# Performance work log

Measured on AMD Instinct MI355X. Metric: run time of the kernel, lower is better.

The kernel has to match this reference:

```python
import jax, jax.numpy as jnp
import numpy as np

N = 50000      # nodes
E = 800000     # edges (avg degree 16)
F_IN = 64      # node_features (== GENConv out, so no input projection)
H = 64         # hidden
EXP = 2 * H    # GENConv MLP expansion dim = 128
D2 = F_IN + H  # dense-block concat dim = SAGEConv in = 128
EPS_MSG = 1e-7 # GENConv message eps
BN_EPS = 1e-5


def setup_inputs() -> dict:
    key = jax.random.key(0)
    ks = jax.random.split(key, 16)
    g = lambda k, shape, fan: jax.random.normal(k, shape, jnp.float32) / np.sqrt(fan)
    return {
        "x": jax.random.normal(ks[0], (N, F_IN), jnp.float32),
        "edge_index": jax.random.randint(ks[1], (2, E), 0, N, jnp.int32),
        # GENConv MLP: Linear(64,128) -> BatchNorm(128) -> ReLU -> Linear(128,64)
        "W1": g(ks[2], (H, EXP), H), "b1": jnp.zeros((EXP,), jnp.float32),
        "gamma": jnp.ones((EXP,), jnp.float32), "beta": jnp.zeros((EXP,), jnp.float32),
        "W2": g(ks[3], (EXP, H), EXP), "b2": jnp.zeros((H,), jnp.float32),
        # SAGEConv project Linear(128,128), lin_l Linear(128,64), lin_r Linear(128,64,bias=False)
        "Wp": g(ks[4], (D2, D2), D2), "bp": jnp.zeros((D2,), jnp.float32),
        "Wl": g(ks[5], (D2, H), D2), "bl": jnp.zeros((H,), jnp.float32),
        "Wr": g(ks[6], (D2, H), D2),
        # fc Linear(64,1)
        "Wf": g(ks[7], (H, 1), H), "bf": jnp.zeros((1,), jnp.float32),
    }


def _forward(x, W1, b1, gamma, beta, W2, b2, Wp, bp, Wl, bl, Wr, Wf, bf, src, dst):
    n = x.shape[0]
    # ---- GENConv(aggr='softmax', t=1.0): msg = relu(x_j) + eps -------------
    msg = jax.nn.relu(x[src]) + EPS_MSG                       # [E, H]
    mmax = jax.ops.segment_max(msg, dst, num_segments=n)      # per-dst, per-feature max
    mmax = jax.lax.stop_gradient(jnp.where(jnp.isfinite(mmax), mmax, 0.0))
    e = jnp.exp(msg - mmax[dst])                              # t = 1.0
    denom = jax.ops.segment_sum(e, dst, num_segments=n)
    numer = jax.ops.segment_sum(e * msg, dst, num_segments=n)
    agg = numer / jnp.where(denom > 0, denom, 1.0)            # softmax aggregation
    out = agg + x                                             # residual with x_dst
    # GENConv MLP (BatchNorm in training mode: batch stats, biased var)
    h = out @ W1 + b1
    mu = h.mean(axis=0)
    var = h.var(axis=0)
    h = (h - mu) * jax.lax.rsqrt(var + BN_EPS) * gamma + beta
    h = jax.nn.relu(h) @ W2 + b2                              # [N, H]
    # ---- DeepGCNLayer block='dense': concat input ---------------------------
    x2 = jnp.concatenate([x, h], axis=-1)                     # [N, F_IN+H]
    x2 = jax.nn.sigmoid(x2)                                   # self.relu = Sigmoid()
    # ---- SAGEConv(project=True, aggr=DeepSetsAggregation()==sum) -----------
    xp = jax.nn.relu(x2 @ Wp + bp)                            # projected source feats
    aggr = jax.ops.segment_sum(xp[src], dst, num_segments=n)  # DeepSets w/o nns = sum
    out2 = aggr @ Wl + bl + x2 @ Wr                           # root uses UNprojected x2
    out2 = jax.nn.sigmoid(out2)
    logits = out2 @ Wf + bf                                   # [N, 1]
    probs = jax.nn.sigmoid(logits)                            # training branch
    return probs, logits


def reference(x, edge_index, W1, b1, gamma, beta, W2, b2, Wp, bp, Wl, bl, Wr, Wf, bf):
    src, dst = edge_index[0], edge_index[1]
    return _forward(x, W1, b1, gamma, beta, W2, b2, Wp, bp, Wl, bl, Wr, Wf, bf, src, dst)
```

## Files before the change

### kernel.cpp

```cpp
#include <hip/hip_runtime.h>

#define F_IN 64
#define HID 64
#define EXPD 128
#define D2 128
#define MAXDEG 64
#define NBW 128
#define NB 391
#define NBINB 98
#define SUBCAP 64
#define EPT 32

typedef __attribute__((ext_vector_type(8))) short bf16x8;
typedef __attribute__((ext_vector_type(4))) float f32x4;

__device__ __forceinline__ float sigmoidf_(float x) {
    return 1.0f / (1.0f + __expf(-x));
}
__device__ __forceinline__ unsigned bf16rne_(float f) {
    unsigned u = __float_as_uint(f);
    return (u + 0x7FFFu + ((u >> 16) & 1u)) >> 16;
}
__device__ __forceinline__ float bf16tof_(unsigned u16) {
    return __uint_as_float(u16 << 16);
}

__global__ __launch_bounds__(256) void k_bin(const int* __restrict__ ei,
                                             int* __restrict__ cnt2,
                                             unsigned* __restrict__ binned2,
                                             const float* __restrict__ x,
                                             unsigned short* __restrict__ x16,
                                             const float* __restrict__ W1,
                                             const float* __restrict__ W2,
                                             const float* __restrict__ Wp,
                                             const float* __restrict__ Wl,
                                             const float* __restrict__ Wr,
                                             short* __restrict__ dst,
                                             float* __restrict__ bnsums,
                                             int nE, int n, int nbinb) {
    int b = blockIdx.x;
    int tid = threadIdx.x;
    if (b < nbinb) {
        __shared__ int hist[NB];
        if (b == 0) bnsums[tid] = 0.f;
        for (int i = tid; i < NB; i += 256) hist[i] = 0;
        __syncthreads();
        unsigned ed[EPT];
        unsigned short rk[EPT];
        int e0 = b * (256 * EPT);
#pragma unroll
        for (int j = 0; j < EPT; ++j) {
            int e = e0 + j * 256 + tid;
            if (e < nE) {
                unsigned s = (unsigned)ei[e];
                unsigned d = (unsigned)ei[nE + e];
                ed[j] = s | (d << 16);
                rk[j] = (unsigned short)atomicAdd(&hist[d >> 7], 1);
            }
        }
        __syncthreads();
        for (int i = tid; i < NB; i += 256) cnt2[b * NB + i] = hist[i];
#pragma unroll
        for (int j = 0; j < EPT; ++j) {
            int e = e0 + j * 256 + tid;
            if (e < nE) {
                int bin = (ed[j] >> 16) >> 7;
                int r = (int)rk[j];
                if (r < SUBCAP)
                    binned2[((size_t)bin * nbinb + b) * SUBCAP + r] = ed[j];
            }
        }
        return;
    }
    b -= nbinb;
    if (b < 192) {
        int e = b * 256 + tid;
        const float* src;
        int K, N, base2;
        if (e < 8192)       { src = W1; K = 64;  N = 128; base2 = 0; }
        else if (e < 16384) { src = W2; K = 128; N = 64;  base2 = 8192; }
        else if (e < 32768) { src = Wp; K = 128; N = 128; base2 = 16384; }
        else if (e < 40960) { src = Wl; K = 128; N = 64;  base2 = 32768; }
        else                { src = Wr; K = 128; N = 64;  base2 = 40960; }
        int le = e - base2;
        int j = le & 7;
        int lane = (le >> 3) & 63;
        int n16 = lane & 15, q = lane >> 4;
        int rest = le >> 9;
        int KC = K / 32;
        int kc = rest % KC, nt = rest / KC;
        int k = kc * 32 + q * 8 + j;
        int col = nt * 16 + n16;
        dst[e] = (short)bf16rne_(src[(size_t)k * N + col]);
        return;
    }
    int i0 = (b - 192) * 1024 + tid * 4;
    if (i0 < n * F_IN) {
        float4 v = *(const float4*)(x + i0);
        uint2 pk;
        pk.x = bf16rne_(v.x) | (bf16rne_(v.y) << 16);
        pk.y = bf16rne_(v.z) | (bf16rne_(v.w) << 16);
        *(uint2*)(x16 + i0) = pk;
    }
}

__global__ __launch_bounds__(256) void k_csr(const int* __restrict__ cnt2,
                                             const unsigned* __restrict__ binned2,
                                             int* __restrict__ counts,
                                             unsigned short* __restrict__ csr,
                                             int n, int nbinb) {
    __shared__ unsigned short lcsr[NBW * MAXDEG];
    __shared__ int lcnt[NBW];
    __shared__ int scnt[NBINB];
    int b = blockIdx.x;
    int tid = threadIdx.x;
    if (tid < NBW) lcnt[tid] = 0;
    for (int i = tid; i < nbinb; i += 256) {
        int c = cnt2[i * NB + b];
        scnt[i] = c < SUBCAP ? c : SUBCAP;
    }
    __syncthreads();
    const unsigned* src = binned2 + (size_t)b * nbinb * SUBCAP;
    int tot = nbinb * SUBCAP;
    for (int i = tid; i < tot; i += 256) {
        int blk = i >> 6;
        int r = i & (SUBCAP - 1);
        if (r < scnt[blk]) {
            unsigned u = src[i];
            int dl = (int)(u >> 16) - b * NBW;
            int slot = atomicAdd(&lcnt[dl], 1);
            if (slot < MAXDEG) lcsr[dl * MAXDEG + slot] = (unsigned short)(u & 0xFFFF);
        }
    }
    __syncthreads();
    int nodebase = b * NBW;
    if (tid < NBW && nodebase + tid < n) counts[nodebase + tid] = lcnt[tid];
    int nrows = n - nodebase;
    nrows = nrows < NBW ? nrows : NBW;
    int nu4 = nrows * 8;
    uint4* dstrow = (uint4*)(csr + (size_t)nodebase * MAXDEG);
    for (int idx = tid; idx < nu4; idx += 256) dstrow[idx] = ((const uint4*)lcsr)[idx];
}

__global__ __launch_bounds__(1024) void k_geng(const unsigned short* __restrict__ x16,
                                               const int* __restrict__ counts,
                                               const unsigned short* __restrict__ csr,
                                               const short* __restrict__ Wf,
                                               const float* __restrict__ b1,
                                               unsigned short* __restrict__ h16,
                                               float* __restrict__ bnsums, int n) {
    __shared__ short As[64 * 64];
    __shared__ float bnred[256];
    const unsigned* x32 = (const unsigned*)x16;
    int tid = threadIdx.x;
    int w = tid >> 6;
    int lane = tid & 63;
    int H = lane >> 5, f2 = lane & 31;
    int rblk = blockIdx.x * 64;
    if (tid < 256) bnred[tid] = 0.f;
    for (int t = 0; t < 4; ++t) {
        int rr = w * 4 + t;
        int v = rblk + rr;
        int q8 = f2 >> 2;
        int slot = ((rr >> 4) * 2 + (q8 >> 2)) * 64 + (q8 & 3) * 16 + (rr & 15);
        if (v < n) {
            int deg = counts[v];
            deg = deg > MAXDEG ? MAXDEG : deg;
            int idx = 0;
            if (lane < deg) idx = (int)csr[(size_t)v * MAXDEG + lane];
            float d0 = 0.f, d1 = 0.f, n0 = 0.f, n1 = 0.f;
            int i = 0;
            for (; i + 16 <= deg; i += 16) {
                unsigned us[8];
#pragma unroll
                for (int tt = 0; tt < 8; ++tt) {
                    int s = __shfl(idx, i + tt * 2 + H, 64);
                    us[tt] = x32[(size_t)s * 32 + f2];
                }
#pragma unroll
                for (int tt = 0; tt < 8; ++tt) {
                    unsigned u = us[tt];
                    float m0 = fmaxf(bf16tof_(u & 0xFFFF), 0.f) + 1e-7f;
                    float m1 = fmaxf(bf16tof_(u >> 16), 0.f) + 1e-7f;
                    float e0 = __expf(m0), e1 = __expf(m1);
                    d0 += e0; d1 += e1;
                    n0 = fmaf(e0, m0, n0);
                    n1 = fmaf(e1, m1, n1);
                }
            }
            for (; i + 8 <= deg; i += 8) {
                int sA = __shfl(idx, i + 0 + H, 64);
                int sB = __shfl(idx, i + 2 + H, 64);
                int sC = __shfl(idx, i + 4 + H, 64);
                int sD = __shfl(idx, i + 6 + H, 64);
                unsigned uA = x32[(size_t)sA * 32 + f2];
                unsigned uB = x32[(size_t)sB * 32 + f2];
                unsigned uC = x32[(size_t)sC * 32 + f2];
                unsigned uD = x32[(size_t)sD * 32 + f2];
#pragma unroll
                for (int tt = 0; tt < 4; ++tt) {
                    unsigned u = tt == 0 ? uA : tt == 1 ? uB : tt == 2 ? uC : uD;
                    float m0 = fmaxf(bf16tof_(u & 0xFFFF), 0.f) + 1e-7f;
                    float m1 = fmaxf(bf16tof_(u >> 16), 0.f) + 1e-7f;
                    float e0 = __expf(m0), e1 = __expf(m1);
                    d0 += e0; d1 += e1;
                    n0 = fmaf(e0, m0, n0);
                    n1 = fmaf(e1, m1, n1);
                }
            }
            for (; i + 2 <= deg; i += 2) {
                int s = __shfl(idx, i + H, 64);
                unsigned u = x32[(size_t)s * 32 + f2];
                float m0 = fmaxf(bf16tof_(u & 0xFFFF), 0.f) + 1e-7f;
                float m1 = fmaxf(bf16tof_(u >> 16), 0.f) + 1e-7f;
                float e0 = __expf(m0), e1 = __expf(m1);
                d0 += e0; d1 += e1;
                n0 = fmaf(e0, m0, n0);
                n1 = fmaf(e1, m1, n1);
            }
            if (i < deg) {
                int s = __shfl(idx, i, 64);
                if (H == 0) {
                    unsigned u = x32[(size_t)s * 32 + f2];
                    float m0 = fmaxf(bf16tof_(u & 0xFFFF), 0.f) + 1e-7f;
                    float m1 = fmaxf(bf16tof_(u >> 16), 0.f) + 1e-7f;
                    float e0 = __expf(m0), e1 = __expf(m1);
                    d0 += e0; d1 += e1;
                    n0 = fmaf(e0, m0, n0);
                    n1 = fmaf(e1, m1, n1);
                }
            }
            d0 += __shfl_xor(d0, 32, 64);
            d1 += __shfl_xor(d1, 32, 64);
            n0 += __shfl_xor(n0, 32, 64);
            n1 += __shfl_xor(n1, 32, 64);
            if (H == 0) {
                float a0 = (deg > 0) ? (n0 / d0) : 0.f;
                float a1 = (deg > 0) ? (n1 / d1) : 0.f;
                unsigned xv = x32[(size_t)v * 32 + f2];
                float r0 = a0 + bf16tof_(xv & 0xFFFF);
                float r1 = a1 + bf16tof_(xv >> 16);
                *(unsigned*)(As + slot * 8 + (f2 & 3) * 2) =
                    bf16rne_(r0) | (bf16rne_(r1) << 16);
            }
        } else {
            if (H == 0) *(unsigned*)(As + slot * 8 + (f2 & 3) * 2) = 0u;
        }
    }
    __syncthreads();
    int L = lane;
    int q = L >> 4, n16 = L & 15;
    int mt = w & 3;
    int nt_base = (w >> 2) * 2;
    f32x4 acc[2];
#pragma unroll
    for (int nt = 0; nt < 2; ++nt) acc[nt] = (f32x4){0.f, 0.f, 0.f, 0.f};
#pragma unroll
    for (int kc = 0; kc < 2; ++kc) {
        bf16x8 a = *(const bf16x8*)(As + ((mt * 2 + kc) * 64 + L) * 8);
#pragma unroll
        for (int nt = 0; nt < 2; ++nt) {
            bf16x8 b = *(const bf16x8*)(Wf + (size_t)(((nt_base + nt) * 2 + kc) * 64 + L) * 8);
            acc[nt] = __builtin_amdgcn_mfma_f32_16x16x32_bf16(a, b, acc[nt], 0, 0, 0);
        }
    }
#pragma unroll
    for (int nt = 0; nt < 2; ++nt) {
        int col = (nt_base + nt) * 16 + n16;
        float bv = b1[col];
        float s = 0.f, s2 = 0.f;
#pragma unroll
        for (int r = 0; r < 4; ++r) {
            int row = rblk + mt * 16 + q * 4 + r;
            float hv = acc[nt][r] + bv;
            if (row < n) {
                h16[(size_t)row * EXPD + col] = (unsigned short)bf16rne_(hv);
                s += hv;
                s2 = fmaf(hv, hv, s2);
            }
        }
        s += __shfl_xor(s, 16, 64);
        s += __shfl_xor(s, 32, 64);
        s2 += __shfl_xor(s2, 16, 64);
        s2 += __shfl_xor(s2, 32, 64);
        if (q == 0) {
            atomicAdd(&bnred[col], s);
            atomicAdd(&bnred[128 + col], s2);
        }
    }
    __syncthreads();
    if (tid < 256) atomicAdd(&bnsums[tid], bnred[tid]);
}

__global__ __launch_bounds__(256) void k_mlp2ab(const unsigned short* __restrict__ h16,
                                                const float* __restrict__ bnsums,
                                                const float* __restrict__ gamma,
                                                const float* __restrict__ beta,
                                                const short* __restrict__ Wf2,
                                                const float* __restrict__ b2,
                                                const unsigned short* __restrict__ x16,
                                                const short* __restrict__ Wfp,
                                                const short* __restrict__ Wfl,
                                                const short* __restrict__ Wfr,
                                                const float* __restrict__ bp,
                                                unsigned short* __restrict__ yp16,
                                                unsigned short* __restrict__ yr16,
                                                float inv_n, int n) {
    __shared__ short Bs[64 * 128];
    __shared__ short As[64 * 128];
    __shared__ float ssl[256];
    int tid = threadIdx.x;
    int rblk = blockIdx.x * 64;
    if (tid < 128) {
        float mu = bnsums[tid] * inv_n;
        float var = fmaf(-mu, mu, bnsums[128 + tid] * inv_n);
        float rs = rsqrtf(fmaxf(var, 0.f) + 1e-5f);
        float scale = gamma[tid] * rs;
        ssl[tid] = scale;
        ssl[128 + tid] = fmaf(-mu, scale, beta[tid]);
    }
    __syncthreads();
#pragma unroll
    for (int it = 0; it < 4; ++it) {
        int c = it * 256 + tid;
        int rr = c & 63, q8 = c >> 6;
        int gr = rblk + rr;
        gr = gr < n ? gr : n - 1;
        uint4 v = *(const uint4*)(h16 + (size_t)gr * EXPD + q8 * 8);
        float4 sc1 = *(const float4*)(ssl + q8 * 8);
        float4 sc2 = *(const float4*)(ssl + q8 * 8 + 4);
        float4 sh1 = *(const float4*)(ssl + 128 + q8 * 8);
        float4 sh2 = *(const float4*)(ssl + 128 + q8 * 8 + 4);
        float o0 = fmaxf(fmaf(bf16tof_(v.x & 0xFFFF), sc1.x, sh1.x), 0.f);
        float o1 = fmaxf(fmaf(bf16tof_(v.x >> 16),    sc1.y, sh1.y), 0.f);
        float o2 = fmaxf(fmaf(bf16tof_(v.y & 0xFFFF), sc1.z, sh1.z), 0.f);
        float o3 = fmaxf(fmaf(bf16tof_(v.y >> 16),    sc1.w, sh1.w), 0.f);
        float o4 = fmaxf(fmaf(bf16tof_(v.z & 0xFFFF), sc2.x, sh2.x), 0.f);
        float o5 = fmaxf(fmaf(bf16tof_(v.z >> 16),    sc2.y, sh2.y), 0.f);
        float o6 = fmaxf(fmaf(bf16tof_(v.w & 0xFFFF), sc2.z, sh2.z), 0.f);
        float o7 = fmaxf(fmaf(bf16tof_(v.w >> 16),    sc2.w, sh2.w), 0.f);
        uint4 pk;
        pk.x = bf16rne_(o0) | (bf16rne_(o1) << 16);
        pk.y = bf16rne_(o2) | (bf16rne_(o3) << 16);
        pk.z = bf16rne_(o4) | (bf16rne_(o5) << 16);
        pk.w = bf16rne_(o6) | (bf16rne_(o7) << 16);
        int slot = ((rr >> 4) * 4 + (q8 >> 2)) * 64 + (q8 & 3) * 16 + (rr & 15);
        *(uint4*)(Bs + slot * 8) = pk;
    }
#pragma unroll
    for (int it = 0; it < 2; ++it) {
        int c = it * 256 + tid;
        int rr = c & 63, q8 = c >> 6;
        int gr = rblk + rr;
        gr = gr < n ? gr : n - 1;
        uint4 v = *(const uint4*)(x16 + (size_t)gr * F_IN + q8 * 8);
        float o0 = sigmoidf_(bf16tof_(v.x & 0xFFFF));
        float o1 = sigmoidf_(bf16tof_(v.x >> 16));
        float o2 = sigmoidf_(bf16tof_(v.y & 0xFFFF));
        float o3 = sigmoidf_(bf16tof_(v.y >> 16));
        float o4 = sigmoidf_(bf16tof_(v.z & 0xFFFF));
        float o5 = sigmoidf_(bf16tof_(v.z >> 16));
        float o6 = sigmoidf_(bf16tof_(v.w & 0xFFFF));
        float o7 = sigmoidf_(bf16tof_(v.w >> 16));
        uint4 pk;
        pk.x = bf16rne_(o0) | (bf16rne_(o1) << 16);
        pk.y = bf16rne_(o2) | (bf16rne_(o3) << 16);
        pk.z = bf16rne_(o4) | (bf16rne_(o5) << 16);
        pk.w = bf16rne_(o6) | (bf16rne_(o7) << 16);
        int slot = ((rr >> 4) * 4 + (q8 >> 2)) * 64 + (q8 & 3) * 16 + (rr & 15);
        *(uint4*)(As + slot * 8) = pk;
    }
    __syncthreads();
    int L = tid & 63, w = tid >> 6;
    int q = L >> 4, n16 = L & 15;
    {
        int mtb = (w & 1) * 2, ntb = (w >> 1) * 2;
        f32x4 acch[2][2];
#pragma unroll
        for (int mt = 0; mt < 2; ++mt)
#pragma unroll
            for (int nt = 0; nt < 2; ++nt) acch[mt][nt] = (f32x4){0.f, 0.f, 0.f, 0.f};
#pragma unroll
        for (int kc = 0; kc < 4; ++kc) {
            bf16x8 a0 = *(const bf16x8*)(Bs + (((mtb + 0) * 4 + kc) * 64 + L) * 8);
            bf16x8 a1 = *(const bf16x8*)(Bs + (((mtb + 1) * 4 + kc) * 64 + L) * 8);
#pragma unroll
            for (int nt = 0; nt < 2; ++nt) {
                bf16x8 b = *(const bf16x8*)(Wf2 + (size_t)(((ntb + nt) * 4 + kc) * 64 + L) * 8);
                acch[0][nt] = __builtin_amdgcn_mfma_f32_16x16x32_bf16(a0, b, acch[0][nt], 0, 0, 0);
                acch[1][nt] = __builtin_amdgcn_mfma_f32_16x16x32_bf16(a1, b, acch[1][nt], 0, 0, 0);
            }
        }
#pragma unroll
        for (int nt = 0; nt < 2; ++nt) {
            int col = (ntb + nt) * 16 + n16;
            float bv = b2[col];
            int q8b = 8 + (col >> 3), jb = col & 7;
#pragma unroll
            for (int mt = 0; mt < 2; ++mt)
#pragma unroll
                for (int r = 0; r < 4; ++r) {
                    int rr2 = (w & 1) * 32 + mt * 16 + q * 4 + r;
                    float hv = sigmoidf_(acch[mt][nt][r] + bv);
                    int slot = ((rr2 >> 4) * 4 + (q8b >> 2)) * 64 + (q8b & 3) * 16 + (rr2 & 15);
                    As[slot * 8 + jb] = (short)bf16rne_(hv);
                }
        }
    }
    __syncthreads();
    int mt_base = (w & 1) * 2;
    int nt_base = (w >> 1) * 4;
    f32x4 acc[2][4];
    f32x4 accr[2][2];
#pragma unroll
    for (int mt = 0; mt < 2; ++mt) {
#pragma unroll
        for (int nt = 0; nt < 4; ++nt) acc[mt][nt] = (f32x4){0.f, 0.f, 0.f, 0.f};
#pragma unroll
        for (int nt = 0; nt < 2; ++nt) accr[mt][nt] = (f32x4){0.f, 0.f, 0.f, 0.f};
    }
#pragma unroll
    for (int kc = 0; kc < 4; ++kc) {
        bf16x8 a0 = *(const bf16x8*)(As + (((mt_base + 0) * 4 + kc) * 64 + L) * 8);
        bf16x8 a1 = *(const bf16x8*)(As + (((mt_base + 1) * 4 + kc) * 64 + L) * 8);
#pragma unroll
        for (int nt = 0; nt < 4; ++nt) {
            bf16x8 b = *(const bf16x8*)(Wfp + (size_t)(((nt_base + nt) * 4 + kc) * 64 + L) * 8);
            acc[0][nt] = __builtin_amdgcn_mfma_f32_16x16x32_bf16(a0, b, acc[0][nt], 0, 0, 0);
            acc[1][nt] = __builtin_amdgcn_mfma_f32_16x16x32_bf16(a1, b, acc[1][nt], 0, 0, 0);
        }
#pragma unroll
        for (int nt = 0; nt < 2; ++nt) {
            bf16x8 b = *(const bf16x8*)(Wfr + (size_t)((((w >> 1) * 2 + nt) * 4 + kc) * 64 + L) * 8);
            accr[0][nt] = __builtin_amdgcn_mfma_f32_16x16x32_bf16(a0, b, accr[0][nt], 0, 0, 0);
            accr[1][nt] = __builtin_amdgcn_mfma_f32_16x16x32_bf16(a1, b, accr[1][nt], 0, 0, 0);
        }
    }
#pragma unroll
    for (int nt = 0; nt < 2; ++nt) {
        int col = ((w >> 1) * 2 + nt) * 16 + n16;
#pragma unroll
        for (int mt = 0; mt < 2; ++mt)
#pragma unroll
            for (int r = 0; r < 4; ++r) {
                int row = rblk + (w & 1) * 32 + mt * 16 + q * 4 + r;
                if (row < n)
                    yr16[(size_t)row * HID + col] = (unsigned short)bf16rne_(accr[mt][nt][r]);
            }
    }
#pragma unroll
    for (int nt = 0; nt < 4; ++nt) {
        int kk = (nt_base + nt) * 16 + n16;
        float bv = bp[kk];
        int q8b = kk >> 3, jb = kk & 7;
#pragma unroll
        for (int mt = 0; mt < 2; ++mt)
#pragma unroll
            for (int r = 0; r < 4; ++r) {
                int rr2 = (w & 1) * 32 + mt * 16 + q * 4 + r;
                float xv = fmaxf(acc[mt][nt][r] + bv, 0.f);
                int slot = ((rr2 >> 4) * 4 + (q8b >> 2)) * 64 + (q8b & 3) * 16 + (rr2 & 15);
                Bs[slot * 8 + jb] = (short)bf16rne_(xv);
            }
    }
    __syncthreads();
    f32x4 acc2[4];
#pragma unroll
    for (int nt = 0; nt < 4; ++nt) acc2[nt] = (f32x4){0.f, 0.f, 0.f, 0.f};
#pragma unroll
    for (int kc = 0; kc < 4; ++kc) {
        bf16x8 a = *(const bf16x8*)(Bs + ((w * 4 + kc) * 64 + L) * 8);
#pragma unroll
        for (int nt = 0; nt < 4; ++nt) {
            bf16x8 b = *(const bf16x8*)(Wfl + (size_t)((nt * 4 + kc) * 64 + L) * 8);
            acc2[nt] = __builtin_amdgcn_mfma_f32_16x16x32_bf16(a, b, acc2[nt], 0, 0, 0);
        }
    }
#pragma unroll
    for (int nt = 0; nt < 4; ++nt) {
        int col = nt * 16 + n16;
#pragma unroll
        for (int r = 0; r < 4; ++r) {
            int row = rblk + w * 16 + q * 4 + r;
            if (row < n)
                yp16[(size_t)row * HID + col] = (unsigned short)bf16rne_(acc2[nt][r]);
        }
    }
}

__global__ __launch_bounds__(256) void k_sagef(const unsigned short* __restrict__ yp16,
                                               const int* __restrict__ counts,
                                               const unsigned short* __restrict__ csr,
                                               const unsigned short* __restrict__ yr16,
                                               const float* __restrict__ bl,
                                               const float* __restrict__ Wfv,
                                               const float* __restrict__ bf,
                                               float* __restrict__ out, int n) {
    const unsigned* yp32 = (const unsigned*)yp16;
    int wid = threadIdx.x >> 6;
    int lane = threadIdx.x & 63;
    int H = lane >> 5, f2 = lane & 31;
    int v = blockIdx.x * 4 + wid;
    if (v >= n) return;
    int deg = counts[v];
    deg = deg > MAXDEG ? MAXDEG : deg;
    int idx = 0;
    if (lane < deg) idx = (int)csr[(size_t)v * MAXDEG + lane];
    float a0 = 0.f, a1 = 0.f;
    int i = 0;
    for (; i + 16 <= deg; i += 16) {
        unsigned us[8];
#pragma unroll
        for (int tt = 0; tt < 8; ++tt) {
            int s = __shfl(idx, i + tt * 2 + H, 64);
            us[tt] = yp32[(size_t)s * 32 + f2];
        }
#pragma unroll
        for (int tt = 0; tt < 8; ++tt) {
            a0 += bf16tof_(us[tt] & 0xFFFF);
            a1 += bf16tof_(us[tt] >> 16);
        }
    }
    for (; i + 8 <= deg; i += 8) {
        int sA = __shfl(idx, i + 0 + H, 64);
        int sB = __shfl(idx, i + 2 + H, 64);
        int sC = __shfl(idx, i + 4 + H, 64);
        int sD = __shfl(idx, i + 6 + H, 64);
        unsigned uA = yp32[(size_t)sA * 32 + f2];
        unsigned uB = yp32[(size_t)sB * 32 + f2];
        unsigned uC = yp32[(size_t)sC * 32 + f2];
        unsigned uD = yp32[(size_t)sD * 32 + f2];
        a0 += bf16tof_(uA & 0xFFFF) + bf16tof_(uB & 0xFFFF) +
              bf16tof_(uC & 0xFFFF) + bf16tof_(uD & 0xFFFF);
        a1 += bf16tof_(uA >> 16) + bf16tof_(uB >> 16) +
              bf16tof_(uC >> 16) + bf16tof_(uD >> 16);
    }
    for (; i + 2 <= deg; i += 2) {
        int s = __shfl(idx, i + H, 64);
        unsigned u = yp32[(size_t)s * 32 + f2];
        a0 += bf16tof_(u & 0xFFFF);
        a1 += bf16tof_(u >> 16);
    }
    if (i < deg) {
        int s = __shfl(idx, i, 64);
        if (H == 0) {
            unsigned u = yp32[(size_t)s * 32 + f2];
            a0 += bf16tof_(u & 0xFFFF);
            a1 += bf16tof_(u >> 16);
        }
    }
    a0 += __shfl_xor(a0, 32, 64);
    a1 += __shfl_xor(a1, 32, 64);
    if (H == 0) {
        unsigned u = ((const unsigned*)yr16)[(size_t)v * 32 + f2];
        float2 blv = ((const float2*)bl)[f2];
        float2 wv  = ((const float2*)Wfv)[f2];
        float o0 = sigmoidf_(a0 + blv.x + bf16tof_(u & 0xFFFF));
        float o1 = sigmoidf_(a1 + blv.y + bf16tof_(u >> 16));
        float t = fmaf(o0, wv.x, o1 * wv.y);
        t += __shfl_xor(t, 1, 64);
        t += __shfl_xor(t, 2, 64);
        t += __shfl_xor(t, 4, 64);
        t += __shfl_xor(t, 8, 64);
        t += __shfl_xor(t, 16, 64);
        if (f2 == 0) {
            float lg = t + bf[0];
            out[v] = sigmoidf_(lg);
            out[n + v] = lg;
        }
    }
}

extern "C" void kernel_launch(void* const* d_in, const int* in_sizes, int n_in,
                              void* d_out, int out_size, void* d_ws, size_t ws_size,
                              hipStream_t stream) {
    const float* x     = (const float*)d_in[0];
    const int*   ei    = (const int*)d_in[1];
    const float* W1    = (const float*)d_in[2];
    const float* b1    = (const float*)d_in[3];
    const float* gamma = (const float*)d_in[4];
    const float* beta  = (const float*)d_in[5];
    const float* W2    = (const float*)d_in[6];
    const float* b2    = (const float*)d_in[7];
    const float* Wp    = (const float*)d_in[8];
    const float* bp    = (const float*)d_in[9];
    const float* Wl    = (const float*)d_in[10];
    const float* bl    = (const float*)d_in[11];
    const float* Wr    = (const float*)d_in[12];
    const float* Wfv   = (const float*)d_in[13];
    const float* bf    = (const float*)d_in[14];
    const int n = in_sizes[0] / F_IN;
    const int e = in_sizes[1] / 2;

    char* ws = (char*)d_ws;
    size_t off = 0;
    auto alloc = [&](size_t bytes) -> void* {
        void* p = (void*)(ws + off);
        off += (bytes + 255) & ~(size_t)255;
        return p;
    };
    const int nbinb = (e + 256 * EPT - 1) / (256 * EPT);
    float*          bnsums   = (float*)alloc(256 * 4);
    int*            cnt2     = (int*)alloc((size_t)nbinb * NB * 4);
    int*            counts   = (int*)alloc((size_t)n * 4);
    unsigned short* csr      = (unsigned short*)alloc((size_t)n * MAXDEG * 2);
    unsigned*       binned2  = (unsigned*)alloc((size_t)NB * nbinb * SUBCAP * 4);
    unsigned short* x16      = (unsigned short*)alloc((size_t)n * F_IN * 2);
    unsigned short* h16      = (unsigned short*)alloc((size_t)n * EXPD * 2);
    unsigned short* yp16     = (unsigned short*)alloc((size_t)n * HID * 2);
    unsigned short* yr16     = (unsigned short*)alloc((size_t)n * HID * 2);
    short*          wfrag    = (short*)alloc(49152 * 2);

    float* out = (float*)d_out;
    const int nb64  = (n + 63) / 64;
    const int nb4   = (n + 3) / 4;
    const int nfp = nbinb + 192 + ((n * F_IN + 1023) / 1024);

    k_bin<<<nfp, 256, 0, stream>>>(ei, cnt2, binned2, x, x16, W1, W2, Wp, Wl,
                                   Wr, wfrag, bnsums, e, n, nbinb);
    k_csr<<<NB, 256, 0, stream>>>(cnt2, binned2, counts, csr, n, nbinb);
    k_geng<<<nb64, 1024, 0, stream>>>(x16, counts, csr, wfrag, b1, h16, bnsums, n);
    k_mlp2ab<<<nb64, 256, 0, stream>>>(h16, bnsums, gamma, beta, wfrag + 8192, b2,
                                       x16, wfrag + 16384, wfrag + 32768,
                                       wfrag + 40960, bp, yp16, yr16,
                                       1.0f / (float)n, n);
    k_sagef<<<nb4, 256, 0, stream>>>(yp16, counts, csr, yr16, bl, Wfv, bf, out, n);
}
```

Before: 209.5 us.

## Fuse CSR construction into GENConv gather kernel using 64-node bins

Removes the separate k_csr kernel. Each 64-row k_geng block now builds its own node neighbor lists in shared memory from the binned edge buckets, reads degrees and sources from LDS, and also writes counts and CSR out for the later SAGE kernel. Bin width drops from 128 to 64 nodes so the bins line up with the GEMM row blocks, and the per-sub-bucket capacity shrinks from 64 to 40. This saves one launch and the CSR global round trip before the gather. In exchange the gather kernel carries extra shared memory and work before it starts, and a sub-bucket that overflows 40 entries would silently drop edges.

```diff
diff --git a/kernel.cpp b/kernel.cpp
--- a/kernel.cpp
+++ b/kernel.cpp
@@ -5,10 +5,9 @@
 #define EXPD 128
 #define D2 128
 #define MAXDEG 64
-#define NBW 128
-#define NB 391
+#define NB 782
 #define NBINB 98
-#define SUBCAP 64
+#define SUBCAP 40
 #define EPT 32
 
 typedef __attribute__((ext_vector_type(8))) short bf16x8;
@@ -55,7 +54,7 @@
                 unsigned s = (unsigned)ei[e];
                 unsigned d = (unsigned)ei[nE + e];
                 ed[j] = s | (d << 16);
-                rk[j] = (unsigned short)atomicAdd(&hist[d >> 7], 1);
+                rk[j] = (unsigned short)atomicAdd(&hist[d >> 6], 1);
             }
         }
         __syncthreads();
@@ -64,7 +63,7 @@
         for (int j = 0; j < EPT; ++j) {
             int e = e0 + j * 256 + tid;
             if (e < nE) {
-                int bin = (ed[j] >> 16) >> 7;
+                int bin = (ed[j] >> 16) >> 6;
                 int r = (int)rk[j];
                 if (r < SUBCAP)
                     binned2[((size_t)bin * nbinb + b) * SUBCAP + r] = ed[j];
@@ -104,51 +103,19 @@
     }
 }
 
-__global__ __launch_bounds__(256) void k_csr(const int* __restrict__ cnt2,
-                                             const unsigned* __restrict__ binned2,
-                                             int* __restrict__ counts,
-                                             unsigned short* __restrict__ csr,
-                                             int n, int nbinb) {
-    __shared__ unsigned short lcsr[NBW * MAXDEG];
-    __shared__ int lcnt[NBW];
-    __shared__ int scnt[NBINB];
-    int b = blockIdx.x;
-    int tid = threadIdx.x;
-    if (tid < NBW) lcnt[tid] = 0;
-    for (int i = tid; i < nbinb; i += 256) {
-        int c = cnt2[i * NB + b];
-        scnt[i] = c < SUBCAP ? c : SUBCAP;
-    }
-    __syncthreads();
-    const unsigned* src = binned2 + (size_t)b * nbinb * SUBCAP;
-    int tot = nbinb * SUBCAP;
-    for (int i = tid; i < tot; i += 256) {
-        int blk = i >> 6;
-        int r = i & (SUBCAP - 1);
-        if (r < scnt[blk]) {
-            unsigned u = src[i];
-            int dl = (int)(u >> 16) - b * NBW;
-            int slot = atomicAdd(&lcnt[dl], 1);
-            if (slot < MAXDEG) lcsr[dl * MAXDEG + slot] = (unsigned short)(u & 0xFFFF);
-        }
-    }
-    __syncthreads();
-    int nodebase = b * NBW;
-    if (tid < NBW && nodebase + tid < n) counts[nodebase + tid] = lcnt[tid];
-    int nrows = n - nodebase;
-    nrows = nrows < NBW ? nrows : NBW;
-    int nu4 = nrows * 8;
-    uint4* dstrow = (uint4*)(csr + (size_t)nodebase * MAXDEG);
-    for (int idx = tid; idx < nu4; idx += 256) dstrow[idx] = ((const uint4*)lcsr)[idx];
-}
-
-__global__ __launch_bounds__(1024) void k_geng(const unsigned short* __restrict__ x16,
-                                               const int* __restrict__ counts,
-                                               const unsigned short* __restrict__ csr,
+__global__ __launch_bounds__(1024) void k_geng(const int* __restrict__ cnt2,
+                                               const unsigned* __restrict__ binned2,
+                                               const unsigned short* __restrict__ x16,
                                                const short* __restrict__ Wf,
                                                const float* __restrict__ b1,
                                                unsigned short* __restrict__ h16,
-                                               float* __restrict__ bnsums, int n) {
+                                               float* __restrict__ bnsums,
+                                               int* __restrict__ counts,
+                                               unsigned short* __restrict__ csr,
+                                               int n, int nbinb) {
+    __shared__ unsigned short lcsr[64 * MAXDEG];
+    __shared__ int lcnt[64];
+    __shared__ int scnt[NBINB];
     __shared__ short As[64 * 64];
     __shared__ float bnred[256];
     const unsigned* x32 = (const unsigned*)x16;
@@ -156,18 +123,46 @@
     int w = tid >> 6;
     int lane = tid & 63;
     int H = lane >> 5, f2 = lane & 31;
-    int rblk = blockIdx.x * 64;
+    int b = blockIdx.x;
+    int rblk = b * 64;
+    if (tid < 64) lcnt[tid] = 0;
     if (tid < 256) bnred[tid] = 0.f;
+    for (int i = tid; i < nbinb; i += 1024) {
+        int c = cnt2[i * NB + b];
+        scnt[i] = c < SUBCAP ? c : SUBCAP;
+    }
+    __syncthreads();
+    const unsigned* esrc = binned2 + (size_t)b * nbinb * SUBCAP;
+    int tot = nbinb * SUBCAP;
+    for (int i = tid; i < tot; i += 1024) {
+        int blk = i / SUBCAP;
+        int r = i - blk * SUBCAP;
+        if (r < scnt[blk]) {
+            unsigned u = esrc[i];
+            int dl = (int)(u >> 16) - rblk;
+            int slot = atomicAdd(&lcnt[dl], 1);
+            if (slot < MAXDEG) lcsr[dl * MAXDEG + slot] = (unsigned short)(u & 0xFFFF);
+        }
+    }
+    __syncthreads();
+    if (tid < 64 && rblk + tid < n) counts[rblk + tid] = lcnt[tid];
+    {
+        int nrows = n - rblk;
+        nrows = nrows < 64 ? nrows : 64;
+        int nu4 = nrows * 8;
+        uint4* dstrow = (uint4*)(csr + (size_t)rblk * MAXDEG);
+        for (int i = tid; i < nu4; i += 1024) dstrow[i] = ((const uint4*)lcsr)[i];
+    }
     for (int t = 0; t < 4; ++t) {
         int rr = w * 4 + t;
         int v = rblk + rr;
         int q8 = f2 >> 2;
         int slot = ((rr >> 4) * 2 + (q8 >> 2)) * 64 + (q8 & 3) * 16 + (rr & 15);
         if (v < n) {
-            int deg = counts[v];
+            int deg = lcnt[rr];
             deg = deg > MAXDEG ? MAXDEG : deg;
             int idx = 0;
-            if (lane < deg) idx = (int)csr[(size_t)v * MAXDEG + lane];
+            if (lane < deg) idx = (int)lcsr[rr * MAXDEG + lane];
             float d0 = 0.f, d1 = 0.f, n0 = 0.f, n1 = 0.f;
             int i = 0;
             for (; i + 16 <= deg; i += 16) {
@@ -260,8 +255,8 @@
         bf16x8 a = *(const bf16x8*)(As + ((mt * 2 + kc) * 64 + L) * 8);
 #pragma unroll
         for (int nt = 0; nt < 2; ++nt) {
-            bf16x8 b = *(const bf16x8*)(Wf + (size_t)(((nt_base + nt) * 2 + kc) * 64 + L) * 8);
-            acc[nt] = __builtin_amdgcn_mfma_f32_16x16x32_bf16(a, b, acc[nt], 0, 0, 0);
+            bf16x8 b2 = *(const bf16x8*)(Wf + (size_t)(((nt_base + nt) * 2 + kc) * 64 + L) * 8);
+            acc[nt] = __builtin_amdgcn_mfma_f32_16x16x32_bf16(a, b2, acc[nt], 0, 0, 0);
         }
     }
 #pragma unroll
@@ -618,8 +613,8 @@
 
     k_bin<<<nfp, 256, 0, stream>>>(ei, cnt2, binned2, x, x16, W1, W2, Wp, Wl,
                                    Wr, wfrag, bnsums, e, n, nbinb);
-    k_csr<<<NB, 256, 0, stream>>>(cnt2, binned2, counts, csr, n, nbinb);
-    k_geng<<<nb64, 1024, 0, stream>>>(x16, counts, csr, wfrag, b1, h16, bnsums, n);
+    k_geng<<<nb64, 1024, 0, stream>>>(cnt2, binned2, x16, wfrag, b1, h16, bnsums,
+                                      counts, csr, n, nbinb);
     k_mlp2ab<<<nb64, 256, 0, stream>>>(h16, bnsums, gamma, beta, wfrag + 8192, b2,
                                        x16, wfrag + 16384, wfrag + 32768,
                                        wfrag + 40960, bp, yp16, yr16,
```

Result: faster. 199.9 us (median of 2 runs) (-4.6%).
